# Kernel tuning notes

Hardware: AMD Instinct MI355X
Metric: run time of the kernel (lower is better)

## Reference

```python
import jax, jax.numpy as jnp
import numpy as np

T = 1024
B = 64
A = 128
ABSTRACT_PENALTY = 0.5
CONSISTENCY_RATIO = 1.0
NEG = -1e30  # acts as log(0) mask; exp underflows to exactly 0 in logsumexp
STOP_IX, CONT_IX = 0, 1


def setup_inputs() -> dict:
    key = jax.random.key(0)
    k1, k2, k3, k4, k5 = jax.random.split(key, 5)
    actions = jax.random.randint(k1, (T,), 0, A, dtype=jnp.int32)
    action_logps = jax.nn.log_softmax(jax.random.normal(k2, (T + 1, B, A), dtype=jnp.float32), axis=-1)
    stop_logps = jax.nn.log_softmax(jax.random.normal(k3, (T + 1, B, 2), dtype=jnp.float32), axis=-1)
    start_logps = jax.nn.log_softmax(jax.random.normal(k4, (T + 1, B), dtype=jnp.float32), axis=-1)
    consistency_penalties = -0.1 * jnp.abs(jax.random.normal(k5, (T + 1, T + 1, B), dtype=jnp.float32))
    return {
        'actions': actions,
        'action_logps': action_logps,
        'stop_logps': stop_logps,
        'start_logps': start_logps,
        'consistency_penalties': consistency_penalties,
    }


def _hsmm_loss(actions, action_logps, stop_logps, start_logps, consistency_penalties):
    T_ = actions.shape[0]
    b = start_logps.shape[1]
    # option_step_dist as fixed (T, b) buffer, rows > current step masked to NEG
    dist0 = jnp.full((T_, b), NEG, dtype=action_logps.dtype).at[0].set(start_logps[0])
    # step i=0: only the action logp (no stop/start rearrange, no consistency pen)
    logp0 = jax.nn.logsumexp(dist0 + action_logps[0, :, actions[0]][None, :])

    idx = jnp.arange(1, T_)
    stop_lps = stop_logps[1:T_, :, STOP_IX]          # (T-1, b)
    cont_lps = stop_logps[1:T_, :, CONT_IX]          # (T-1, b)
    start_lps = start_logps[1:T_]                    # (T-1, b)
    act_lps = action_logps[idx, :, actions[1:]]      # (T-1, b)
    # column i of consistency_penalties, rows :T (masked dist rows kill rows > i)
    cons_cols = jnp.transpose(consistency_penalties[:T_, 1:T_, :], (1, 0, 2))  # (T-1, T, b)

    def step(carry, xs):
        dist, logp, cons = carry
        i, stop_lp, cont_lp, start_lp, act_lp, cp = xs
        total_rearrange = jax.nn.logsumexp(dist + stop_lp[None, :]) - ABSTRACT_PENALTY
        new_mass = start_lp + total_rearrange
        dist = (dist + cont_lp[None, :]).at[i].set(new_mass)
        cons = cons + jax.nn.logsumexp(dist + cp)
        logp = logp + jax.nn.logsumexp(dist + act_lp[None, :])
        return (dist, logp, cons), None

    init = (dist0, logp0, jnp.zeros((), dist0.dtype))
    (dist, logp, cons), _ = jax.lax.scan(step, init, (idx, stop_lps, cont_lps, start_lps, act_lps, cons_cols))
    total_logp = logp + jax.nn.logsumexp(dist + stop_logps[T_, :, STOP_IX][None, :])
    return -total_logp + CONSISTENCY_RATIO * cons


def reference(actions, action_logps, stop_logps, start_logps, consistency_penalties):
    return _hsmm_loss(actions, action_logps, stop_logps, start_logps, consistency_penalties)
```

## Files before the change

### kernel.cpp

```cpp
#include <hip/hip_runtime.h>

#define T_N 1024
#define B_N 64
#define A_N 128
#define TP1 1025

typedef float f32x4 __attribute__((ext_vector_type(4)));

__device__ __forceinline__ float bcf(int x){ return __builtin_bit_cast(float, x); }
__device__ __forceinline__ int   bci(float x){ return __builtin_bit_cast(int, x); }

template<int CTRL, int RM>
__device__ __forceinline__ float dpp_add_step(float x){
  int t = __builtin_amdgcn_update_dpp(0, bci(x), CTRL, RM, 0xf, true);
  return x + bcf(t);
}
__device__ __forceinline__ float wave_sum64(float x){
  x = dpp_add_step<0x111,0xf>(x);
  x = dpp_add_step<0x112,0xf>(x);
  x = dpp_add_step<0x114,0xf>(x);
  x = dpp_add_step<0x118,0xf>(x);
  x = dpp_add_step<0x142,0xa>(x);
  x = dpp_add_step<0x143,0xc>(x);
  return bcf(__builtin_amdgcn_readlane(bci(x), 63));
}
__device__ __forceinline__ void wave_sum64_x4(float a, float b, float c, float d,
                                              float& ra, float& rb, float& rc, float& rd){
  a = dpp_add_step<0x111,0xf>(a); b = dpp_add_step<0x111,0xf>(b);
  c = dpp_add_step<0x111,0xf>(c); d = dpp_add_step<0x111,0xf>(d);
  a = dpp_add_step<0x112,0xf>(a); b = dpp_add_step<0x112,0xf>(b);
  c = dpp_add_step<0x112,0xf>(c); d = dpp_add_step<0x112,0xf>(d);
  a = dpp_add_step<0x114,0xf>(a); b = dpp_add_step<0x114,0xf>(b);
  c = dpp_add_step<0x114,0xf>(c); d = dpp_add_step<0x114,0xf>(d);
  a = dpp_add_step<0x118,0xf>(a); b = dpp_add_step<0x118,0xf>(b);
  c = dpp_add_step<0x118,0xf>(c); d = dpp_add_step<0x118,0xf>(d);
  a = dpp_add_step<0x142,0xa>(a); b = dpp_add_step<0x142,0xa>(b);
  c = dpp_add_step<0x142,0xa>(c); d = dpp_add_step<0x142,0xa>(d);
  a = dpp_add_step<0x143,0xc>(a); b = dpp_add_step<0x143,0xc>(b);
  c = dpp_add_step<0x143,0xc>(c); d = dpp_add_step<0x143,0xc>(d);
  ra = bcf(__builtin_amdgcn_readlane(bci(a), 63));
  rb = bcf(__builtin_amdgcn_readlane(bci(b), 63));
  rc = bcf(__builtin_amdgcn_readlane(bci(c), 63));
  rd = bcf(__builtin_amdgcn_readlane(bci(d), 63));
}
__device__ __forceinline__ float group16_sum(float x){
  x = dpp_add_step<0x111,0xf>(x);
  x = dpp_add_step<0x112,0xf>(x);
  x = dpp_add_step<0x114,0xf>(x);
  x = dpp_add_step<0x118,0xf>(x);
  return x;
}
template<int CTRL, int RM>
__device__ __forceinline__ float dpp_max_step(float x){
  int t = __builtin_amdgcn_update_dpp(bci(-3.4e38f), bci(x), CTRL, RM, 0xf, false);
  return fmaxf(x, bcf(t));
}
__device__ __forceinline__ float wave_max64(float x){
  x = dpp_max_step<0x111,0xf>(x);
  x = dpp_max_step<0x112,0xf>(x);
  x = dpp_max_step<0x114,0xf>(x);
  x = dpp_max_step<0x118,0xf>(x);
  x = dpp_max_step<0x142,0xa>(x);
  x = dpp_max_step<0x143,0xc>(x);
  return bcf(__builtin_amdgcn_readlane(bci(x), 63));
}

__global__ __launch_bounds__(64) void prep_kernel(
    const float* __restrict__ stop_logps,
    const float* __restrict__ start_logps,
    float* __restrict__ quadQ,
    float* __restrict__ cs32,
    float* __restrict__ A1p)
{
  const int bid  = (int)blockIdx.x;
  const int lane = (int)threadIdx.x;
  const float KAPPA = 0.60653065971263342f;
  const float2* stop2 = (const float2*)stop_logps;

  int g = bid * 64 + lane;
  A1p[g] = 0.f; A1p[g + 16384] = 0.f; A1p[g + 32768] = 0.f; A1p[g + 49152] = 0.f;

  if (bid < 255) {
    const int i1 = 4 * bid + 1;
    float2 q1 = stop2[(i1 + 0) * B_N + lane];
    float2 q2 = stop2[(i1 + 1) * B_N + lane];
    float2 q3 = stop2[(i1 + 2) * B_N + lane];
    float2 q4 = stop2[(i1 + 3) * B_N + lane];
    float t1 = start_logps[(i1 + 0) * B_N + lane];
    float t2 = start_logps[(i1 + 1) * B_N + lane];
    float t3 = start_logps[(i1 + 2) * B_N + lane];
    float t4 = start_logps[(i1 + 3) * B_N + lane];
    float e1 = __expf(q1.x), c1 = __expf(q1.y), s1 = KAPPA * __expf(t1);
    float e2 = __expf(q2.x), c2 = __expf(q2.y), s2 = KAPPA * __expf(t2);
    float e3 = __expf(q3.x), c3 = __expf(q3.y), s3 = KAPPA * __expf(t3);
    float e4 = __expf(q4.x), c4 = __expf(q4.y), s4 = KAPPA * __expf(t4);

    float c21  = c2 * c1;
    float c321 = c3 * c21;
    float V1 = e1;
    float V2 = e2 * c1;
    float V3 = e3 * c21;
    float V4 = e4 * c321;

    float Cq = c4 * c321;
    float S1 = c4 * c3 * c2 * s1;
    float S2 = c4 * c3 * s2;
    float S3 = c4 * s3;
    float S4 = s4;

    float k21 = wave_sum64(e2 * s1);
    float k31 = wave_sum64(e3 * c2 * s1);
    float k32 = wave_sum64(e3 * s2);
    float k41 = wave_sum64(e4 * c3 * c2 * s1);
    float k42 = wave_sum64(e4 * c3 * s2);
    float k43 = wave_sum64(e4 * s3);

    float m21 = k21, m32 = k32, m43 = k43;
    float m31 = __builtin_fmaf(k32, k21, k31);
    float m42 = __builtin_fmaf(k43, k32, k42);
    float m41 = __builtin_fmaf(k43, m31, __builtin_fmaf(k42, k21, k41));

    float T4 = S4;
    float T3 = __builtin_fmaf(S4, m43, S3);
    float T2 = __builtin_fmaf(S4, m42, __builtin_fmaf(S3, m32, S2));
    float T1 = __builtin_fmaf(S4, m41,
               __builtin_fmaf(S3, m31, __builtin_fmaf(S2, m21, S1)));

    f32x4* qs = (f32x4*)quadQ;
    size_t base = (size_t)bid * 4 * 64 + lane;
    qs[base + 0 * 64] = (f32x4){V1, V2, V3, V4};
    qs[base + 1 * 64] = (f32x4){Cq, T1, T2, T3};
    qs[base + 2 * 64] = (f32x4){T4, m21, m31, m32};
    qs[base + 3 * 64] = (f32x4){m41, m42, m43, 0.f};
  }

  if (bid < 32) {
    float s = 0.f;
    for (int k = 1; k <= 32; ++k) {
      int i = 32 * bid + k;
      if (i <= 1023) s += stop2[i * B_N + lane].y;
    }
    cs32[bid * B_N + lane] = s;
  }
}

__global__ __launch_bounds__(64, 1) void scan_kernel(
    const float* __restrict__ stop_logps,
    const float* __restrict__ start_logps,
    const float* __restrict__ quadQ,
    float* __restrict__ z_ws,
    float* __restrict__ r_ws,
    float* __restrict__ wexp)
{
  const int lane = threadIdx.x;
  const float2* stop2 = (const float2*)stop_logps;

  float2 sct0 = stop2[1021 * B_N + lane];
  float2 sct1 = stop2[1022 * B_N + lane];
  float2 sct2 = stop2[1023 * B_N + lane];
  float stt0 = start_logps[1021 * B_N + lane];
  float stt1 = start_logps[1022 * B_N + lane];
  float stt2 = start_logps[1023 * B_N + lane];

  float z = __expf(start_logps[lane]);

  const f32x4* qs = (const f32x4*)quadQ;

  f32x4 qb[8][4];
  #pragma unroll
  for (int q = 0; q < 8; ++q)
    #pragma unroll
    for (int s = 0; s < 4; ++s)
      qb[q][s] = qs[((size_t)q * 4 + s) * 64 + lane];

  for (int p0 = 0; p0 < 248; p0 += 8) {
    #pragma unroll
    for (int q = 0; q < 8; ++q) {
      const int p = p0 + q;
      f32x4 V = qb[q][0];
      f32x4 Z = qb[q][1];
      f32x4 W = qb[q][2];
      f32x4 X = qb[q][3];
      {
        const int pn = p + 8;
        #pragma unroll
        for (int s = 0; s < 4; ++s)
          qb[q][s] = qs[((size_t)pn * 4 + s) * 64 + lane];
      }

      float d1, d2, d3, d4;
      wave_sum64_x4(z * V.x, z * V.y, z * V.z, z * V.w, d1, d2, d3, d4);

      float r1 = d1;
      float r2 = __builtin_fmaf(W.y, d1, d2);
      float r3 = __builtin_fmaf(W.w, d2, __builtin_fmaf(W.z, d1, d3));
      float r4 = __builtin_fmaf(X.z, d3,
                 __builtin_fmaf(X.y, d2, __builtin_fmaf(X.x, d1, d4)));
      if (lane == 0) *(f32x4*)(r_ws + 4 * p) = (f32x4){r1, r2, r3, r4};

      float p1 = __builtin_fmaf(d2, Z.z, __builtin_fmaf(d1, Z.y, z * Z.x));
      float p2 = __builtin_fmaf(d4, W.x, d3 * Z.w);
      z = p1 + p2;

      if ((q & 3) == 3) {
        int rb  = bci(r4);
        int e16 = ((rb >> 23) & 255) - 127;
        z = ldexpf(z, -e16);
        if (lane == 0) wexp[p >> 2] = (float)e16;
        if (q == 7)
          z_ws[(4 * p + 4) * B_N + lane] = z;
      }
    }
  }
  #pragma unroll
  for (int q = 0; q < 7; ++q) {
    const int p = 248 + q;
    f32x4 V = qb[q][0];
    f32x4 Z = qb[q][1];
    f32x4 W = qb[q][2];
    f32x4 X = qb[q][3];
    float d1, d2, d3, d4;
    wave_sum64_x4(z * V.x, z * V.y, z * V.z, z * V.w, d1, d2, d3, d4);
    float r1 = d1;
    float r2 = __builtin_fmaf(W.y, d1, d2);
    float r3 = __builtin_fmaf(W.w, d2, __builtin_fmaf(W.z, d1, d3));
    float r4 = __builtin_fmaf(X.z, d3,
               __builtin_fmaf(X.y, d2, __builtin_fmaf(X.x, d1, d4)));
    if (lane == 0) *(f32x4*)(r_ws + 4 * p) = (f32x4){r1, r2, r3, r4};
    float p1 = __builtin_fmaf(d2, Z.z, __builtin_fmaf(d1, Z.y, z * Z.x));
    float p2 = __builtin_fmaf(d4, W.x, d3 * Z.w);
    z = p1 + p2;
    if (q == 3) {
      int rb  = bci(r4);
      int e16 = ((rb >> 23) & 255) - 127;
      z = ldexpf(z, -e16);
      if (lane == 0) wexp[62] = (float)e16;
    }
  }
  const float KAPPA = 0.60653065971263342f;
  {
    float esw = __expf(sct0.x), ecw = __expf(sct0.y), sv = KAPPA * __expf(stt0);
    float r = wave_sum64(z * esw);
    z = __builtin_fmaf(sv, r, z * ecw);
    if (lane == 0) r_ws[1020] = r;
  }
  {
    float esw = __expf(sct1.x), ecw = __expf(sct1.y), sv = KAPPA * __expf(stt1);
    float r = wave_sum64(z * esw);
    z = __builtin_fmaf(sv, r, z * ecw);
    if (lane == 0) r_ws[1021] = r;
  }
  {
    float esw = __expf(sct2.x), ecw = __expf(sct2.y), sv = KAPPA * __expf(stt2);
    float r = wave_sum64(z * esw);
    z = __builtin_fmaf(sv, r, z * ecw);
    if (lane == 0) r_ws[1022] = r;
  }
}

__global__ __launch_bounds__(64) void post_kernel(
    const int* __restrict__ actions,
    const float* __restrict__ action_logps,
    const float* __restrict__ stop_logps,
    const float* __restrict__ start_logps,
    const float* __restrict__ z_ws,
    const float* __restrict__ r_ws,
    const float* __restrict__ wexp,
    const float* __restrict__ cs32,
    float* __restrict__ u_ws,
    float* __restrict__ D_ws,
    float* __restrict__ out)
{
  const int w    = (int)blockIdx.x;
  const int lane = (int)threadIdx.x;
  const float LN2   = 0.69314718055994531f;
  const float KAPPA = 0.60653065971263342f;
  const float2* stop2 = (const float2*)stop_logps;

  float wl = (lane < 63) ? wexp[lane] : 0.f;

  float Pv = LN2 * wave_sum64((lane < 2 * w) ? wl : 0.f);
  float e0 = bcf(__builtin_amdgcn_readlane(bci(wl), 2 * w));

  float C = 0.f;
  for (int c = 0; c < w; ++c) C += cs32[c * B_N + lane];

  float z;
  if (w == 0) {
    z = __expf(start_logps[lane]);
    u_ws[lane] = start_logps[lane];
  } else {
    z = z_ws[(32 * w) * B_N + lane];
  }

  for (int k = 1; k <= 32; ++k) {
    int i = 32 * w + k;
    if (i > 1023) break;
    float cont = stop2[i * B_N + lane].y;
    float stv  = start_logps[i * B_N + lane];
    float r    = r_ws[i - 1];
    C += cont;
    float ecw = __expf(cont);
    float sv  = KAPPA * __expf(stv);
    z = __builtin_fmaf(r, sv, ecw * z);
    float zs = wave_sum64(z);
    float R  = __logf(r) + Pv - 0.5f;
    u_ws[i * B_N + lane] = stv + R - C;
    D_ws[i * B_N + lane] = C - (__logf(zs) + Pv);
    if (k == 16) { z = ldexpf(z, -(int)e0); Pv += LN2 * e0; }
  }

  if (w == 31) {
    float st0 = start_logps[lane];
    int   a0  = actions[0];
    float al0 = action_logps[lane * A_N + a0];
    float lp0 = __logf(wave_sum64(__expf(st0 + al0)));
    float stopT = stop_logps[(T_N * B_N + lane) * 2 + 0];
    float fin = __logf(wave_sum64(z * __expf(stopT))) + Pv;
    if (lane == 0) out[0] = -(lp0 + fin);
  }
}

__global__ __launch_bounds__(256) void cons_logp_kernel(
    const float* __restrict__ cons_pen,
    const float* __restrict__ u_ws,
    const float* __restrict__ D_ws,
    const int* __restrict__ actions,
    const float* __restrict__ action_logps,
    float* __restrict__ A1p,
    float* __restrict__ LQ)
{
  const int bid  = (int)blockIdx.x;
  const int tid  = (int)threadIdx.x;
  const int lane = tid & 63;
  const int wv   = tid >> 6;

  __shared__ float sm[4][64];
  __shared__ float sa[4][64];

  if (bid < 512) {
    const int bq  = (lane & 15) * 4;
    const int row = lane >> 4;
    #pragma unroll
    for (int t = 0; t < 2; ++t) {
      const int j = t ? (1023 - bid) : bid;
      const float4 u4 = *(const float4*)(u_ws + j * B_N + bq);
      float* dst = A1p + ((j & 63) << 10);
      for (int i0 = j + 4 * wv; i0 <= 1023; i0 += 16) {
        int i  = i0 + row;
        int iL = i > 1023 ? 1023 : i;
        f32x4 cp4 = __builtin_nontemporal_load(
            (const f32x4*)(cons_pen + ((size_t)j * TP1 + iL) * B_N + bq));
        float4 d4  = *(const float4*)(D_ws + (size_t)iL * B_N + bq);
        bool valid = (i >= 1) && (i <= 1023);
        float a0 = u4.x + d4.x + cp4.x;
        float a1 = u4.y + d4.y + cp4.y;
        float a2 = u4.z + d4.z + cp4.z;
        float a3 = u4.w + d4.w + cp4.w;
        a0 = valid ? a0 : -1e30f;
        a1 = valid ? a1 : -1e30f;
        a2 = valid ? a2 : -1e30f;
        a3 = valid ? a3 : -1e30f;
        float sred = (__expf(a0) + __expf(a1)) + (__expf(a2) + __expf(a3));
        sred = group16_sum(sred);
        if (((lane & 15) == 15) && valid) atomicAdd(dst + i, sred);
      }
    }
  } else {
    const int i = 1535 - bid;
    int   ai = actions[i];
    float av = action_logps[((size_t)i * B_N + lane) * A_N + ai];

    float mA = -1e30f, aA = 0.f, mB = -1e30f, aB = 0.f;
    for (int jj = wv; jj <= i; jj += 8) {
      float u0 = u_ws[jj * B_N + lane];
      int   j1 = jj + 4;
      float u1 = (j1 <= i) ? u_ws[j1 * B_N + lane] : -1e30f;
      float n0 = fmaxf(mA, u0);
      aA = aA * __expf(mA - n0) + __expf(u0 - n0);
      mA = n0;
      float n1 = fmaxf(mB, u1);
      aB = aB * __expf(mB - n1) + __expf(u1 - n1);
      mB = n1;
    }
    float m   = fmaxf(mA, mB);
    float acc = aA * __expf(mA - m) + aB * __expf(mB - m);

    sm[wv][lane] = m; sa[wv][lane] = acc;
    __syncthreads();
    if (wv == 0) {
      float m0 = sm[0][lane], m1 = sm[1][lane], m2 = sm[2][lane], m3 = sm[3][lane];
      float M2 = fmaxf(fmaxf(m0, m1), fmaxf(m2, m3));
      float A  = sa[0][lane] * __expf(m0 - M2) + sa[1][lane] * __expf(m1 - M2)
               + sa[2][lane] * __expf(m2 - M2) + sa[3][lane] * __expf(m3 - M2);
      float S  = M2 + __logf(A);
      float val = S + D_ws[(size_t)i * B_N + lane] + av;
      float mx  = wave_max64(val);
      float sum = wave_sum64(__expf(val - mx));
      if (lane == 0) LQ[i] = mx + __logf(sum);
    }
  }
}

__global__ __launch_bounds__(256) void finish_kernel(
    const float* __restrict__ A1p,
    const float* __restrict__ LQ,
    float* __restrict__ out)
{
  const int i = (int)blockIdx.x * 256 + (int)threadIdx.x;
  float v = 0.f;
  if (i >= 1 && i <= 1023) {
    float a = 0.f;
    #pragma unroll 8
    for (int p = 0; p < 64; ++p) a += A1p[(p << 10) + i];
    v = __logf(a) - LQ[i];
  }
  float ws = wave_sum64(v);
  __shared__ float sb[4];
  if ((threadIdx.x & 63) == 0) sb[threadIdx.x >> 6] = ws;
  __syncthreads();
  if (threadIdx.x == 0) atomicAdd(out, sb[0] + sb[1] + sb[2] + sb[3]);
}

extern "C" void kernel_launch(void* const* d_in, const int* in_sizes, int n_in,
                              void* d_out, int out_size, void* d_ws, size_t ws_size,
                              hipStream_t stream) {
  const int*   actions      = (const int*)d_in[0];
  const float* action_logps = (const float*)d_in[1];
  const float* stop_logps   = (const float*)d_in[2];
  const float* start_logps  = (const float*)d_in[3];
  const float* cons_pen     = (const float*)d_in[4];
  float* out = (float*)d_out;

  float* z_ws  = (float*)d_ws;
  float* u_ws  = z_ws + T_N * B_N;
  float* D_ws  = u_ws + T_N * B_N;
  float* A1p   = D_ws + T_N * B_N;
  float* r_ws  = A1p + 64 * 1024;
  float* wexp  = r_ws + T_N;
  float* LQ    = wexp + 64;
  float* cs32  = LQ + T_N;
  float* quadQ = cs32 + 32 * B_N;

  hipLaunchKernelGGL(prep_kernel, dim3(256), dim3(64), 0, stream,
                     stop_logps, start_logps, quadQ, cs32, A1p);
  hipLaunchKernelGGL(scan_kernel, dim3(1), dim3(64), 0, stream,
                     stop_logps, start_logps, quadQ, z_ws, r_ws, wexp);
  hipLaunchKernelGGL(post_kernel, dim3(32), dim3(64), 0, stream,
                     actions, action_logps, stop_logps, start_logps,
                     z_ws, r_ws, wexp, cs32, u_ws, D_ws, out);
  hipLaunchKernelGGL(cons_logp_kernel, dim3(1535), dim3(256), 0, stream,
                     cons_pen, u_ws, D_ws, actions, action_logps, A1p, LQ);
  hipLaunchKernelGGL(finish_kernel, dim3(4), dim3(256), 0, stream,
                     A1p, LQ, out);
}
```

Measured before the change: 463.2 us.

## Prefetch consistency penalties into cache during scan, move r-recovery to post kernel

The single-wave serial scan kernel now launches 255 extra blocks that read the consistency-penalty tensor into a dummy sink, warming the L2/MALL for the later cons_logp kernel while the serial scan runs. The scan drops its per-step r reconstruction and stores raw d values instead, with post_kernel (now 64 blocks of 16 steps each) rebuilding r from quadQ. Loads in cons_logp lose the nontemporal hint so the warmed lines can be reused. Risks: the prefetch blocks may contend with the latency-critical scan wave, and a 64 KB LDS request limits co-residency.

```diff
diff --git a/kernel.cpp b/kernel.cpp
--- a/kernel.cpp
+++ b/kernel.cpp
@@ -69,7 +69,7 @@
     const float* __restrict__ stop_logps,
     const float* __restrict__ start_logps,
     float* __restrict__ quadQ,
-    float* __restrict__ cs32,
+    float* __restrict__ cs16,
     float* __restrict__ A1p)
 {
   const int bid  = (int)blockIdx.x;
@@ -134,25 +134,52 @@
     qs[base + 3 * 64] = (f32x4){m41, m42, m43, 0.f};
   }
 
-  if (bid < 32) {
+  if (bid < 64) {
     float s = 0.f;
-    for (int k = 1; k <= 32; ++k) {
-      int i = 32 * bid + k;
+    for (int k = 1; k <= 16; ++k) {
+      int i = 16 * bid + k;
       if (i <= 1023) s += stop2[i * B_N + lane].y;
     }
-    cs32[bid * B_N + lane] = s;
-  }
-}
-
-__global__ __launch_bounds__(64, 1) void scan_kernel(
+    cs16[bid * B_N + lane] = s;
+  }
+}
+
+__global__ __launch_bounds__(256, 1) void scan_kernel(
     const float* __restrict__ stop_logps,
     const float* __restrict__ start_logps,
     const float* __restrict__ quadQ,
+    const float* __restrict__ cons_pen,
     float* __restrict__ z_ws,
-    float* __restrict__ r_ws,
-    float* __restrict__ wexp)
+    float* __restrict__ d_ws,
+    float* __restrict__ wexp,
+    float* __restrict__ sink)
 {
-  const int lane = threadIdx.x;
+  extern __shared__ float lds_pad[];
+  (void)lds_pad;
+  const int bid = (int)blockIdx.x;
+
+  if (bid != 0) {
+    const int c = bid - 1;
+    float s = 0.f;
+    #pragma unroll
+    for (int t = 0; t < 2; ++t) {
+      const int j = t ? (1023 - c) : c;
+      const f32x4* p4 = (const f32x4*)(cons_pen + ((size_t)j * TP1 + j) * B_N);
+      const int n4 = (1024 - j) * 16;
+      for (int base = 0; base < n4; base += 256 * 8) {
+        #pragma unroll
+        for (int u = 0; u < 8; ++u) {
+          int idx = base + (int)threadIdx.x + 256 * u;
+          if (idx < n4) s += p4[idx].x;
+        }
+      }
+    }
+    sink[bid] = s;
+    return;
+  }
+  if (threadIdx.x >= 64) return;
+
+  const int lane = (int)threadIdx.x;
   const float2* stop2 = (const float2*)stop_logps;
 
   float2 sct0 = stop2[1021 * B_N + lane];
@@ -166,11 +193,11 @@
 
   const f32x4* qs = (const f32x4*)quadQ;
 
-  f32x4 qb[8][4];
+  f32x4 qb[8][3];
   #pragma unroll
   for (int q = 0; q < 8; ++q)
     #pragma unroll
-    for (int s = 0; s < 4; ++s)
+    for (int s = 0; s < 3; ++s)
       qb[q][s] = qs[((size_t)q * 4 + s) * 64 + lane];
 
   for (int p0 = 0; p0 < 248; p0 += 8) {
@@ -180,35 +207,26 @@
       f32x4 V = qb[q][0];
       f32x4 Z = qb[q][1];
       f32x4 W = qb[q][2];
-      f32x4 X = qb[q][3];
       {
         const int pn = p + 8;
         #pragma unroll
-        for (int s = 0; s < 4; ++s)
+        for (int s = 0; s < 3; ++s)
           qb[q][s] = qs[((size_t)pn * 4 + s) * 64 + lane];
       }
 
       float d1, d2, d3, d4;
       wave_sum64_x4(z * V.x, z * V.y, z * V.z, z * V.w, d1, d2, d3, d4);
-
-      float r1 = d1;
-      float r2 = __builtin_fmaf(W.y, d1, d2);
-      float r3 = __builtin_fmaf(W.w, d2, __builtin_fmaf(W.z, d1, d3));
-      float r4 = __builtin_fmaf(X.z, d3,
-                 __builtin_fmaf(X.y, d2, __builtin_fmaf(X.x, d1, d4)));
-      if (lane == 0) *(f32x4*)(r_ws + 4 * p) = (f32x4){r1, r2, r3, r4};
+      if (lane == 0) *(f32x4*)(d_ws + 4 * p) = (f32x4){d1, d2, d3, d4};
 
       float p1 = __builtin_fmaf(d2, Z.z, __builtin_fmaf(d1, Z.y, z * Z.x));
       float p2 = __builtin_fmaf(d4, W.x, d3 * Z.w);
       z = p1 + p2;
 
       if ((q & 3) == 3) {
-        int rb  = bci(r4);
-        int e16 = ((rb >> 23) & 255) - 127;
+        int e16 = ((bci(d4) >> 23) & 255) - 127;
         z = ldexpf(z, -e16);
         if (lane == 0) wexp[p >> 2] = (float)e16;
-        if (q == 7)
-          z_ws[(4 * p + 4) * B_N + lane] = z;
+        z_ws[(4 * p + 4) * B_N + lane] = z;
       }
     }
   }
@@ -218,23 +236,17 @@
     f32x4 V = qb[q][0];
     f32x4 Z = qb[q][1];
     f32x4 W = qb[q][2];
-    f32x4 X = qb[q][3];
     float d1, d2, d3, d4;
     wave_sum64_x4(z * V.x, z * V.y, z * V.z, z * V.w, d1, d2, d3, d4);
-    float r1 = d1;
-    float r2 = __builtin_fmaf(W.y, d1, d2);
-    float r3 = __builtin_fmaf(W.w, d2, __builtin_fmaf(W.z, d1, d3));
-    float r4 = __builtin_fmaf(X.z, d3,
-               __builtin_fmaf(X.y, d2, __builtin_fmaf(X.x, d1, d4)));
-    if (lane == 0) *(f32x4*)(r_ws + 4 * p) = (f32x4){r1, r2, r3, r4};
+    if (lane == 0) *(f32x4*)(d_ws + 4 * p) = (f32x4){d1, d2, d3, d4};
     float p1 = __builtin_fmaf(d2, Z.z, __builtin_fmaf(d1, Z.y, z * Z.x));
     float p2 = __builtin_fmaf(d4, W.x, d3 * Z.w);
     z = p1 + p2;
     if (q == 3) {
-      int rb  = bci(r4);
-      int e16 = ((rb >> 23) & 255) - 127;
+      int e16 = ((bci(d4) >> 23) & 255) - 127;
       z = ldexpf(z, -e16);
       if (lane == 0) wexp[62] = (float)e16;
+      z_ws[1008 * B_N + lane] = z;
     }
   }
   const float KAPPA = 0.60653065971263342f;
@@ -242,19 +254,19 @@
     float esw = __expf(sct0.x), ecw = __expf(sct0.y), sv = KAPPA * __expf(stt0);
     float r = wave_sum64(z * esw);
     z = __builtin_fmaf(sv, r, z * ecw);
-    if (lane == 0) r_ws[1020] = r;
+    if (lane == 0) d_ws[1020] = r;
   }
   {
     float esw = __expf(sct1.x), ecw = __expf(sct1.y), sv = KAPPA * __expf(stt1);
     float r = wave_sum64(z * esw);
     z = __builtin_fmaf(sv, r, z * ecw);
-    if (lane == 0) r_ws[1021] = r;
+    if (lane == 0) d_ws[1021] = r;
   }
   {
     float esw = __expf(sct2.x), ecw = __expf(sct2.y), sv = KAPPA * __expf(stt2);
     float r = wave_sum64(z * esw);
     z = __builtin_fmaf(sv, r, z * ecw);
-    if (lane == 0) r_ws[1022] = r;
+    if (lane == 0) d_ws[1022] = r;
   }
 }
 
@@ -263,10 +275,11 @@
     const float* __restrict__ action_logps,
     const float* __restrict__ stop_logps,
     const float* __restrict__ start_logps,
+    const float* __restrict__ quadQ,
     const float* __restrict__ z_ws,
-    const float* __restrict__ r_ws,
+    const float* __restrict__ d_ws,
     const float* __restrict__ wexp,
-    const float* __restrict__ cs32,
+    const float* __restrict__ cs16,
     float* __restrict__ u_ws,
     float* __restrict__ D_ws,
     float* __restrict__ out)
@@ -276,41 +289,67 @@
   const float LN2   = 0.69314718055994531f;
   const float KAPPA = 0.60653065971263342f;
   const float2* stop2 = (const float2*)stop_logps;
+  const f32x4* qs = (const f32x4*)quadQ;
 
   float wl = (lane < 63) ? wexp[lane] : 0.f;
 
-  float Pv = LN2 * wave_sum64((lane < 2 * w) ? wl : 0.f);
-  float e0 = bcf(__builtin_amdgcn_readlane(bci(wl), 2 * w));
+  float Pv = LN2 * wave_sum64((lane < w) ? wl : 0.f);
 
   float C = 0.f;
-  for (int c = 0; c < w; ++c) C += cs32[c * B_N + lane];
+  for (int c = 0; c < w; ++c) C += cs16[c * B_N + lane];
 
   float z;
   if (w == 0) {
     z = __expf(start_logps[lane]);
     u_ws[lane] = start_logps[lane];
   } else {
-    z = z_ws[(32 * w) * B_N + lane];
-  }
-
-  for (int k = 1; k <= 32; ++k) {
-    int i = 32 * w + k;
-    if (i > 1023) break;
-    float cont = stop2[i * B_N + lane].y;
-    float stv  = start_logps[i * B_N + lane];
-    float r    = r_ws[i - 1];
-    C += cont;
-    float ecw = __expf(cont);
-    float sv  = KAPPA * __expf(stv);
-    z = __builtin_fmaf(r, sv, ecw * z);
-    float zs = wave_sum64(z);
-    float R  = __logf(r) + Pv - 0.5f;
-    u_ws[i * B_N + lane] = stv + R - C;
-    D_ws[i * B_N + lane] = C - (__logf(zs) + Pv);
-    if (k == 16) { z = ldexpf(z, -(int)e0); Pv += LN2 * e0; }
-  }
-
-  if (w == 31) {
+    z = z_ws[(16 * w) * B_N + lane];
+  }
+
+  const int nquad = (w == 63) ? 3 : 4;
+  for (int g = 0; g < nquad; ++g) {
+    const int gq = 4 * w + g;
+    f32x4 Wm = qs[((size_t)gq * 4 + 2) * 64 + lane];
+    f32x4 Xm = qs[((size_t)gq * 4 + 3) * 64 + lane];
+    f32x4 dv = *(const f32x4*)(d_ws + 4 * gq);
+    float r0 = dv.x;
+    float r1 = __builtin_fmaf(Wm.y, dv.x, dv.y);
+    float r2 = __builtin_fmaf(Wm.w, dv.y, __builtin_fmaf(Wm.z, dv.x, dv.z));
+    float r3 = __builtin_fmaf(Xm.z, dv.z,
+               __builtin_fmaf(Xm.y, dv.y, __builtin_fmaf(Xm.x, dv.x, dv.w)));
+    float rq[4] = {r0, r1, r2, r3};
+    #pragma unroll
+    for (int k2 = 0; k2 < 4; ++k2) {
+      int i = 4 * gq + k2 + 1;
+      float cont = stop2[i * B_N + lane].y;
+      float stv  = start_logps[i * B_N + lane];
+      float r    = rq[k2];
+      C += cont;
+      float ecw = __expf(cont);
+      float sv  = KAPPA * __expf(stv);
+      z = __builtin_fmaf(r, sv, ecw * z);
+      float zs = wave_sum64(z);
+      float R  = __logf(r) + Pv - 0.5f;
+      u_ws[i * B_N + lane] = stv + R - C;
+      D_ws[i * B_N + lane] = C - (__logf(zs) + Pv);
+    }
+  }
+  if (w == 63) {
+    #pragma unroll
+    for (int k2 = 0; k2 < 3; ++k2) {
+      int i = 1021 + k2;
+      float cont = stop2[i * B_N + lane].y;
+      float stv  = start_logps[i * B_N + lane];
+      float r    = d_ws[i - 1];
+      C += cont;
+      float ecw = __expf(cont);
+      float sv  = KAPPA * __expf(stv);
+      z = __builtin_fmaf(r, sv, ecw * z);
+      float zs = wave_sum64(z);
+      float R  = __logf(r) + Pv - 0.5f;
+      u_ws[i * B_N + lane] = stv + R - C;
+      D_ws[i * B_N + lane] = C - (__logf(zs) + Pv);
+    }
     float st0 = start_logps[lane];
     int   a0  = actions[0];
     float al0 = action_logps[lane * A_N + a0];
@@ -349,8 +388,7 @@
       for (int i0 = j + 4 * wv; i0 <= 1023; i0 += 16) {
         int i  = i0 + row;
         int iL = i > 1023 ? 1023 : i;
-        f32x4 cp4 = __builtin_nontemporal_load(
-            (const f32x4*)(cons_pen + ((size_t)j * TP1 + iL) * B_N + bq));
+        f32x4 cp4 = *(const f32x4*)(cons_pen + ((size_t)j * TP1 + iL) * B_N + bq);
         float4 d4  = *(const float4*)(D_ws + (size_t)iL * B_N + bq);
         bool valid = (i >= 1) && (i <= 1023);
         float a0 = u4.x + d4.x + cp4.x;
@@ -436,19 +474,21 @@
   float* u_ws  = z_ws + T_N * B_N;
   float* D_ws  = u_ws + T_N * B_N;
   float* A1p   = D_ws + T_N * B_N;
-  float* r_ws  = A1p + 64 * 1024;
-  float* wexp  = r_ws + T_N;
+  float* d_wsv = A1p + 64 * 1024;
+  float* wexp  = d_wsv + T_N;
   float* LQ    = wexp + 64;
-  float* cs32  = LQ + T_N;
-  float* quadQ = cs32 + 32 * B_N;
+  float* cs16  = LQ + T_N;
+  float* quadQ = cs16 + 64 * B_N;
+  float* sink  = quadQ + 256 * 4 * B_N * 4;
 
   hipLaunchKernelGGL(prep_kernel, dim3(256), dim3(64), 0, stream,
-                     stop_logps, start_logps, quadQ, cs32, A1p);
-  hipLaunchKernelGGL(scan_kernel, dim3(1), dim3(64), 0, stream,
-                     stop_logps, start_logps, quadQ, z_ws, r_ws, wexp);
-  hipLaunchKernelGGL(post_kernel, dim3(32), dim3(64), 0, stream,
+                     stop_logps, start_logps, quadQ, cs16, A1p);
+  hipLaunchKernelGGL(scan_kernel, dim3(256), dim3(256), 65536, stream,
+                     stop_logps, start_logps, quadQ, cons_pen,
+                     z_ws, d_wsv, wexp, sink);
+  hipLaunchKernelGGL(post_kernel, dim3(64), dim3(64), 0, stream,
                      actions, action_logps, stop_logps, start_logps,
-                     z_ws, r_ws, wexp, cs32, u_ws, D_ws, out);
+                     quadQ, z_ws, d_wsv, wexp, cs16, u_ws, D_ws, out);
   hipLaunchKernelGGL(cons_logp_kernel, dim3(1535), dim3(256), 0, stream,
                      cons_pen, u_ws, D_ws, actions, action_logps, A1p, LQ);
   hipLaunchKernelGGL(finish_kernel, dim3(4), dim3(256), 0, stream,
```

Result: faster. 449.6 us (-2.9%).
